# Optimization experiments

Measured on AMD Instinct MI355X. Metric: run time of the kernel, lower is better.

The kernel has to match this reference:

```python
import jax, jax.numpy as jnp
import numpy as np
import math

BS, S, D = 1, 2048, 1024
H = 16
DK = D // H  # 64


def _log_sparse_neighbor_mask(seq_len):
    """mask[i,j]=True iff j==i, or j in [i-k, i) with k=seq_len//2, or i-j is a power of 2.
    Matches generate_log_sparse_plus_neighbors_mask(seq_len, seq_len//2)."""
    k = seq_len // 2
    i = jnp.arange(seq_len, dtype=jnp.int32)[:, None]
    j = jnp.arange(seq_len, dtype=jnp.int32)[None, :]
    diff = i - j
    neighbor = (diff >= 0) & (diff <= k)  # includes diagonal (diff==0)
    pow2 = (diff > 0) & ((diff & (diff - 1)) == 0)
    return neighbor | pow2  # [seq_len, seq_len] bool


def setup_inputs() -> dict:
    key = jax.random.key(0)
    ks = jax.random.split(key, 9)
    std = 0.02
    return {
        "Q": jax.random.normal(ks[0], (BS, S, D), dtype=jnp.float32),
        "Wq": jax.random.normal(ks[1], (D, H * DK), dtype=jnp.float32) * std,
        "bq": jnp.zeros((H * DK,), dtype=jnp.float32),
        "Wk": jax.random.normal(ks[2], (D, H * DK), dtype=jnp.float32) * std,
        "bk": jnp.zeros((H * DK,), dtype=jnp.float32),
        "Wv": jax.random.normal(ks[3], (D, H * DK), dtype=jnp.float32) * std,
        "bv": jnp.zeros((H * DK,), dtype=jnp.float32),
        "Wo": jax.random.normal(ks[4], (H * DK, D), dtype=jnp.float32) * std,
        "bo": jnp.zeros((D,), dtype=jnp.float32),
    }


def reference(Q, Wq, bq, Wk, bk, Wv, bv, Wo, bo):
    bs, s, d = Q.shape
    # QKV projections -> [bs, h, s, dk]
    q = (Q @ Wq + bq).reshape(bs, s, H, DK).transpose(0, 2, 1, 3)
    k = (Q @ Wk + bk).reshape(bs, s, H, DK).transpose(0, 2, 1, 3)
    v = (Q @ Wv + bv).reshape(bs, s, H, DK).transpose(0, 2, 1, 3)

    # log_sparse_attention: scale is 1/sqrt(d_k); mask regenerated internally
    mask = _log_sparse_neighbor_mask(s)  # [s, s] bool
    scores = jnp.einsum("bhqd,bhkd->bhqk", q, k) / math.sqrt(DK)
    scores = jnp.where(mask[None, None, :, :], scores, -jnp.inf)
    attn = jax.nn.softmax(scores, axis=-1)  # [bs, h, s, s]
    out = jnp.einsum("bhqk,bhkd->bhqd", attn, v)

    # merge heads + output projection
    out = out.transpose(0, 2, 1, 3).reshape(bs, s, H * DK)
    out = out @ Wo + bo
    return (out, attn)
```

## Files before the change

### kernel.cpp

```cpp
#include <hip/hip_runtime.h>

#define SEQ 2048
#define DM 1024
#define NH 16
#define DKH 64
#define BAND 1024
#define QKV 3072
#define PBW 1064

typedef __attribute__((ext_vector_type(8))) __bf16 bf16x8;
typedef __attribute__((ext_vector_type(4))) __bf16 bf16x4;
typedef __attribute__((ext_vector_type(4))) float f32x4;

static __device__ __forceinline__ f32x4 mfma16(bf16x8 a, bf16x8 b, f32x4 c) {
  return __builtin_amdgcn_mfma_f32_16x16x32_bf16(a, b, c, 0, 0, 0);
}

#define GLOAD16(gp, lp)                                                        \
  __builtin_amdgcn_global_load_lds(                                            \
      (const __attribute__((address_space(1))) void*)(gp),                     \
      (__attribute__((address_space(3))) void*)(lp), 16, 0, 0)

struct PrepArgs {
  const float* win[4];
  __bf16* wout[4];
  const float* Q;
  __bf16* Qb;
};
__global__ void prep(PrepArgs P) {
  int z = blockIdx.z;
  if (z < 4) {
    __shared__ float t[32][33];
    const float* in = P.win[z];
    __bf16* out = P.wout[z];
    int c0 = blockIdx.x * 32, r0 = blockIdx.y * 32;
    int tx = threadIdx.x, ty = threadIdx.y;
    for (int r = ty; r < 32; r += 8)
      t[r][tx] = in[(size_t)(r0 + r) * DM + c0 + tx];
    __syncthreads();
    for (int r = ty; r < 32; r += 8)
      out[(size_t)(c0 + r) * DM + r0 + tx] = (__bf16)t[tx][r];
  } else {
    int t = threadIdx.y * 32 + threadIdx.x;
    int base = (blockIdx.y * 32 + blockIdx.x) * 512 + t;
#pragma unroll
    for (int u = 0; u < 2; u++) {
      int i = base + u * 256;
      float4 v = reinterpret_cast<const float4*>(P.Q)[i];
      bf16x4 o = {(__bf16)v.x, (__bf16)v.y, (__bf16)v.z, (__bf16)v.w};
      reinterpret_cast<bf16x4*>(P.Qb)[i] = o;
    }
  }
}

template <int BM, int BN, bool BF16OUT, bool VOUT>
__global__ __launch_bounds__(256) void gemm_lds(
    const __bf16* __restrict__ A, const __bf16* __restrict__ BT,
    const float* __restrict__ b0, const float* __restrict__ b1,
    const float* __restrict__ b2, float* __restrict__ Cf,
    __bf16* __restrict__ Cb, __bf16* __restrict__ VT, int M, int N, int K) {
  constexpr int BK = 64;
  constexpr int FM = BM / 32;
  constexpr int FN = BN / 32;
  constexpr int LA = BM * BK * 2 / (256 * 16);
  constexpr int LB = BN * BK * 2 / (256 * 16);
  __shared__ __bf16 lA[2][BM * BK];
  __shared__ __bf16 lB[2][BN * BK];
  int tid = threadIdx.x;
  int lane = tid & 63;
  int l15 = lane & 15, lg = lane >> 4;
  int w = tid >> 6;
  int nwg = gridDim.x * gridDim.y;
  int bid = blockIdx.y * gridDim.x + blockIdx.x;
  int swz = (bid & 7) * (nwg >> 3) + (bid >> 3);
  int bx = swz % gridDim.x;
  int by = swz / gridDim.x;
  int row0 = by * BM;
  int col0 = bx * BN;
  int sec = col0 >> 10;
  const float* bias = sec == 0 ? b0 : (sec == 1 ? b1 : b2);
  int cbase = col0 & (DM - 1);
  int wr = (w >> 1) * (BM / 2);
  int wc = (w & 1) * (BN / 2);
  f32x4 acc[FM][FN] = {};

  auto stage = [&](int b, int kt) {
#pragma unroll
    for (int s = 0; s < LA; s++) {
      int u = tid + s * 256;
      int r = u >> 3;
      int cc = (u & 7) ^ (r & 7);
      GLOAD16(A + (size_t)(row0 + r) * K + kt * BK + cc * 8,
              (char*)lA[b] + u * 16);
    }
#pragma unroll
    for (int s = 0; s < LB; s++) {
      int u = tid + s * 256;
      int r = u >> 3;
      int cc = (u & 7) ^ (r & 7);
      GLOAD16(BT + (size_t)(col0 + r) * K + kt * BK + cc * 8,
              (char*)lB[b] + u * 16);
    }
  };

  const int T = K / BK;
  stage(0, 0);
  stage(1, 1);
  for (int t = 0; t < T; t++) {
    if (t + 1 < T)
      asm volatile("s_waitcnt vmcnt(%0)" ::"i"(LA + LB) : "memory");
    else
      asm volatile("s_waitcnt vmcnt(0)" ::: "memory");
    __builtin_amdgcn_s_barrier();
    int cur = t & 1;
    bf16x8 af[2][FM], bfr[2][FN];
#pragma unroll
    for (int kh = 0; kh < 2; kh++) {
#pragma unroll
      for (int mi = 0; mi < FM; mi++) {
        int r = wr + mi * 16 + l15;
        af[kh][mi] = *(const bf16x8*)((const char*)lA[cur] + r * 128 +
                                      ((((kh << 2) | lg) ^ (r & 7)) << 4));
      }
#pragma unroll
      for (int ni = 0; ni < FN; ni++) {
        int r = wc + ni * 16 + l15;
        bfr[kh][ni] = *(const bf16x8*)((const char*)lB[cur] + r * 128 +
                                       ((((kh << 2) | lg) ^ (r & 7)) << 4));
      }
    }
    __builtin_amdgcn_s_setprio(1);
#pragma unroll
    for (int kh = 0; kh < 2; kh++)
#pragma unroll
      for (int mi = 0; mi < FM; mi++)
#pragma unroll
        for (int ni = 0; ni < FN; ni++)
          acc[mi][ni] = mfma16(af[kh][mi], bfr[kh][ni], acc[mi][ni]);
    __builtin_amdgcn_s_setprio(0);
    __builtin_amdgcn_s_barrier();
    if (t + 2 < T) stage(cur, t + 2);
  }

  if (VOUT && sec == 2) {
#pragma unroll
    for (int mi = 0; mi < FM; mi++) {
      int row = row0 + wr + mi * 16 + lg * 4;
#pragma unroll
      for (int ni = 0; ni < FN; ni++) {
        int hd = cbase + wc + ni * 16 + l15;
        float b = bias[hd];
        bf16x4 pk;
#pragma unroll
        for (int r = 0; r < 4; r++) pk[r] = (__bf16)(acc[mi][ni][r] + b);
        *(bf16x4*)&VT[(size_t)hd * SEQ + row] = pk;
      }
    }
    return;
  }
#pragma unroll
  for (int mi = 0; mi < FM; mi++) {
    int row = row0 + wr + mi * 16 + lg * 4;
#pragma unroll
    for (int ni = 0; ni < FN; ni++) {
      int col = col0 + wc + ni * 16 + l15;
      float b = bias[(cbase + wc + ni * 16 + l15) & (DM - 1)];
#pragma unroll
      for (int r = 0; r < 4; r++) {
        float v = acc[mi][ni][r] + b;
        if constexpr (BF16OUT)
          Cb[(size_t)(row + r) * N + col] = (__bf16)v;
        else
          Cf[(size_t)(row + r) * N + col] = v;
      }
    }
  }
}

__global__ __launch_bounds__(256, 4) void attn_fused(
    const __bf16* __restrict__ qkvb, const __bf16* __restrict__ VT,
    float* __restrict__ attn_out, __bf16* __restrict__ pvb) {
  __shared__ __bf16 pbuf[16][PBW];
  __shared__ float wsum[4][16];
  __shared__ float sinv[16];

  int nwg = gridDim.x * gridDim.y;
  int bid = blockIdx.y * gridDim.x + blockIdx.x;
  int swz = (bid & 7) * (nwg >> 3) + (bid >> 3);
  int h = swz / (SEQ / 16);
  int i0 = (swz % (SEQ / 16)) * 16;

  int tid = threadIdx.x, lane = tid & 63, w = tid >> 6;
  int l15 = lane & 15, lg = lane >> 4;

  int jlo = i0 - BAND;
  if (jlo < 0) jlo = 0;
  int ntiles = (i0 + 16 - jlo) >> 4;
  int ktiles = (ntiles + 1) & ~1;
  int n = ntiles * 16;

  const __bf16* qptr = qkvb + (size_t)(i0 + l15) * QKV + h * DKH + lg * 8;
  bf16x8 aq0 = *(const bf16x8*)qptr;
  bf16x8 aq1 = *(const bf16x8*)(qptr + 32);
  const __bf16* kbase = qkvb + DM + h * DKH + lg * 8;

  float sm[4] = {0.f, 0.f, 0.f, 0.f};
  for (int t = w; t < ntiles; t += 4) {
    int jb = jlo + t * 16;
    const __bf16* kptr = kbase + (size_t)(jb + l15) * QKV;
    f32x4 acc = {0.f, 0.f, 0.f, 0.f};
    __builtin_amdgcn_s_setprio(1);
    acc = mfma16(aq0, *(const bf16x8*)kptr, acc);
    acc = mfma16(aq1, *(const bf16x8*)(kptr + 32), acc);
    __builtin_amdgcn_s_setprio(0);
    int col = jb + l15;
    int x = jb - jlo + l15;
#pragma unroll
    for (int r = 0; r < 4; r++) {
      int i = i0 + lg * 4 + r;
      float e = 0.f;
      if (col <= i && i - col <= BAND) {
        e = __expf(acc[r] * 0.125f);
        sm[r] += e;
      }
      pbuf[lg * 4 + r][x] = (__bf16)e;
    }
  }
  if (ktiles != ntiles) pbuf[tid >> 4][n + (tid & 15)] = (__bf16)0.f;
#pragma unroll
  for (int o = 1; o < 16; o <<= 1)
#pragma unroll
    for (int r = 0; r < 4; r++) sm[r] += __shfl_xor(sm[r], o);
  if (l15 == 0)
#pragma unroll
    for (int r = 0; r < 4; r++) wsum[w][lg * 4 + r] = sm[r];
  __syncthreads();
  if (tid < 16)
    sinv[tid] = 1.f / (wsum[0][tid] + wsum[1][tid] + wsum[2][tid] + wsum[3][tid]);
  __syncthreads();

  f32x4* abase = (f32x4*)(attn_out + ((size_t)h * SEQ + i0) * SEQ);
  for (int idx = tid; idx < 16 * (SEQ / 4); idx += 256) {
    int row = idx >> 9;
    int j4 = idx & 511;
    int x = j4 * 4 - jlo;
    bool valid = (unsigned)x < (unsigned)n;
    int xc = valid ? x : 0;
    bf16x4 v4 = *(const bf16x4*)&pbuf[row][xc];
    float inv = valid ? sinv[row] : 0.f;
    f32x4 o = {(float)v4[0] * inv, (float)v4[1] * inv, (float)v4[2] * inv,
               (float)v4[3] * inv};
    __builtin_nontemporal_store(o, abase + idx);
  }

  f32x4 acc = {0.f, 0.f, 0.f, 0.f};
  int d0 = w * 16;
  const __bf16* vtp = VT + ((size_t)h * DKH + d0 + l15) * SEQ;
  for (int kt = 0; kt < ktiles; kt += 2) {
    int kk = kt * 16;
    bf16x8 pa = *(const bf16x8*)&pbuf[l15][kk + lg * 8];
    int jj = jlo + kk + lg * 8;
    bf16x8 vf = {};
    if (jj < SEQ) vf = *(const bf16x8*)(vtp + jj);
    __builtin_amdgcn_s_setprio(1);
    acc = mfma16(pa, vf, acc);
    __builtin_amdgcn_s_setprio(0);
  }
#pragma unroll
  for (int r = 0; r < 4; r++) {
    int row = lg * 4 + r;
    float inv = sinv[row];
    pvb[(size_t)(i0 + row) * DM + h * DKH + d0 + l15] = (__bf16)(acc[r] * inv);
  }
}

extern "C" void kernel_launch(void* const* d_in, const int* in_sizes, int n_in,
                              void* d_out, int out_size, void* d_ws,
                              size_t ws_size, hipStream_t stream) {
  const float* Q = (const float*)d_in[0];
  const float* Wq = (const float*)d_in[1];
  const float* bq = (const float*)d_in[2];
  const float* Wk = (const float*)d_in[3];
  const float* bk = (const float*)d_in[4];
  const float* Wv = (const float*)d_in[5];
  const float* bv = (const float*)d_in[6];
  const float* Wo = (const float*)d_in[7];
  const float* bo = (const float*)d_in[8];
  float* out_proj = (float*)d_out;
  float* attn_out = out_proj + (size_t)SEQ * DM;

  char* ws = (char*)d_ws;
  size_t off = 0;
  auto alloc = [&](size_t bytes) {
    void* p = ws + off;
    off = (off + bytes + 255) & ~(size_t)255;
    return p;
  };
  __bf16* Qb    = (__bf16*)alloc((size_t)SEQ * DM * 2);
  __bf16* WqkvT = (__bf16*)alloc((size_t)QKV * DM * 2);
  __bf16* WoT   = (__bf16*)alloc((size_t)DM * DM * 2);
  __bf16* qkvb  = (__bf16*)alloc((size_t)SEQ * QKV * 2);
  __bf16* VT    = (__bf16*)alloc((size_t)NH * DKH * SEQ * 2);
  __bf16* pvb   = (__bf16*)alloc((size_t)SEQ * DM * 2);

  PrepArgs P;
  P.win[0] = Wq; P.win[1] = Wk; P.win[2] = Wv; P.win[3] = Wo;
  P.wout[0] = WqkvT;
  P.wout[1] = WqkvT + (size_t)DM * DM;
  P.wout[2] = WqkvT + (size_t)2 * DM * DM;
  P.wout[3] = WoT;
  P.Q = Q;
  P.Qb = Qb;
  prep<<<dim3(32, 32, 5), dim3(32, 8), 0, stream>>>(P);

  gemm_lds<64, 128, true, true><<<dim3(QKV / 128, SEQ / 64), 256, 0, stream>>>(
      Qb, WqkvT, bq, bk, bv, nullptr, qkvb, VT, SEQ, QKV, DM);

  attn_fused<<<dim3(SEQ / 16, NH), 256, 0, stream>>>(qkvb, VT, attn_out, pvb);

  gemm_lds<64, 64, false, false><<<dim3(DM / 64, SEQ / 64), 256, 0, stream>>>(
      pvb, WoT, bo, bo, bo, out_proj, nullptr, nullptr, SEQ, DM, DM);
}
```

Measured before the change: 119.7 us.

## Transpose QK MFMA for vector P stores and interleave attn write with PV

```diff
diff --git a/kernel.cpp b/kernel.cpp
--- a/kernel.cpp
+++ b/kernel.cpp
@@ -204,67 +204,64 @@
   bf16x8 aq1 = *(const bf16x8*)(qptr + 32);
   const __bf16* kbase = qkvb + DM + h * DKH + lg * 8;
 
-  float sm[4] = {0.f, 0.f, 0.f, 0.f};
+  int i = i0 + l15;
+  float sm = 0.f;
   for (int t = w; t < ntiles; t += 4) {
     int jb = jlo + t * 16;
     const __bf16* kptr = kbase + (size_t)(jb + l15) * QKV;
     f32x4 acc = {0.f, 0.f, 0.f, 0.f};
     __builtin_amdgcn_s_setprio(1);
-    acc = mfma16(aq0, *(const bf16x8*)kptr, acc);
-    acc = mfma16(aq1, *(const bf16x8*)(kptr + 32), acc);
+    acc = mfma16(*(const bf16x8*)kptr, aq0, acc);
+    acc = mfma16(*(const bf16x8*)(kptr + 32), aq1, acc);
     __builtin_amdgcn_s_setprio(0);
-    int col = jb + l15;
-    int x = jb - jlo + l15;
+    int kcol = jb + lg * 4;
+    bf16x4 pk;
 #pragma unroll
     for (int r = 0; r < 4; r++) {
-      int i = i0 + lg * 4 + r;
+      int j = kcol + r;
       float e = 0.f;
-      if (col <= i && i - col <= BAND) {
-        e = __expf(acc[r] * 0.125f);
-        sm[r] += e;
-      }
-      pbuf[lg * 4 + r][x] = (__bf16)e;
-    }
+      if (j <= i && i - j <= BAND) {
+        e = exp2f(acc[r] * 0.18033688f);
+        sm += e;
+      }
+      pk[r] = (__bf16)e;
+    }
+    *(bf16x4*)&pbuf[l15][jb - jlo + lg * 4] = pk;
   }
   if (ktiles != ntiles) pbuf[tid >> 4][n + (tid & 15)] = (__bf16)0.f;
-#pragma unroll
-  for (int o = 1; o < 16; o <<= 1)
-#pragma unroll
-    for (int r = 0; r < 4; r++) sm[r] += __shfl_xor(sm[r], o);
-  if (l15 == 0)
-#pragma unroll
-    for (int r = 0; r < 4; r++) wsum[w][lg * 4 + r] = sm[r];
+  sm += __shfl_xor(sm, 16);
+  sm += __shfl_xor(sm, 32);
+  if (lane < 16) wsum[w][lane] = sm;
   __syncthreads();
   if (tid < 16)
     sinv[tid] = 1.f / (wsum[0][tid] + wsum[1][tid] + wsum[2][tid] + wsum[3][tid]);
   __syncthreads();
 
   f32x4* abase = (f32x4*)(attn_out + ((size_t)h * SEQ + i0) * SEQ);
-  for (int idx = tid; idx < 16 * (SEQ / 4); idx += 256) {
-    int row = idx >> 9;
-    int j4 = idx & 511;
-    int x = j4 * 4 - jlo;
-    bool valid = (unsigned)x < (unsigned)n;
-    int xc = valid ? x : 0;
-    bf16x4 v4 = *(const bf16x4*)&pbuf[row][xc];
-    float inv = valid ? sinv[row] : 0.f;
-    f32x4 o = {(float)v4[0] * inv, (float)v4[1] * inv, (float)v4[2] * inv,
-               (float)v4[3] * inv};
-    __builtin_nontemporal_store(o, abase + idx);
-  }
-
   f32x4 acc = {0.f, 0.f, 0.f, 0.f};
   int d0 = w * 16;
   const __bf16* vtp = VT + ((size_t)h * DKH + d0 + l15) * SEQ;
-  for (int kt = 0; kt < ktiles; kt += 2) {
-    int kk = kt * 16;
-    bf16x8 pa = *(const bf16x8*)&pbuf[l15][kk + lg * 8];
-    int jj = jlo + kk + lg * 8;
-    bf16x8 vf = {};
-    if (jj < SEQ) vf = *(const bf16x8*)(vtp + jj);
-    __builtin_amdgcn_s_setprio(1);
-    acc = mfma16(pa, vf, acc);
-    __builtin_amdgcn_s_setprio(0);
+  for (int s = 0; s < 33; s++) {
+    if (s < 32) {
+      int idx = tid + s * 256;
+      int row = idx >> 9;
+      int j4 = idx & 511;
+      int x = j4 * 4 - jlo;
+      bool valid = (unsigned)x < (unsigned)n;
+      bf16x4 v4 = *(const bf16x4*)&pbuf[row][valid ? x : 0];
+      float inv = valid ? sinv[row] : 0.f;
+      f32x4 o = {(float)v4[0] * inv, (float)v4[1] * inv, (float)v4[2] * inv,
+                 (float)v4[3] * inv};
+      __builtin_nontemporal_store(o, abase + idx);
+    }
+    if (2 * s < ktiles) {
+      int kk = s * 32;
+      bf16x8 pa = *(const bf16x8*)&pbuf[l15][kk + lg * 8];
+      int jj = jlo + kk + lg * 8;
+      bf16x8 vf = {};
+      if (jj < SEQ) vf = *(const bf16x8*)(vtp + jj);
+      acc = mfma16(pa, vf, acc);
+    }
   }
 #pragma unroll
   for (int r = 0; r < 4; r++) {
```

After: 120.9 us. No clear change (+1.0%).

## Process 32 query rows per attention block to reuse K and V tiles

Applied to the files above, without the earlier changes.

```diff
diff --git a/kernel.cpp b/kernel.cpp
--- a/kernel.cpp
+++ b/kernel.cpp
@@ -6,6 +6,7 @@
 #define DKH 64
 #define BAND 1024
 #define QKV 3072
+#define QBLK 32
 #define PBW 1064
 
 typedef __attribute__((ext_vector_type(8))) __bf16 bf16x8;
@@ -177,70 +178,90 @@
   }
 }
 
-__global__ __launch_bounds__(256, 4) void attn_fused(
+__global__ __launch_bounds__(256, 2) void attn_fused(
     const __bf16* __restrict__ qkvb, const __bf16* __restrict__ VT,
     float* __restrict__ attn_out, __bf16* __restrict__ pvb) {
-  __shared__ __bf16 pbuf[16][PBW];
-  __shared__ float wsum[4][16];
-  __shared__ float sinv[16];
+  __shared__ __bf16 pbuf[QBLK][PBW];
+  __shared__ float wsum[4][QBLK];
+  __shared__ float sinv[QBLK];
 
   int nwg = gridDim.x * gridDim.y;
   int bid = blockIdx.y * gridDim.x + blockIdx.x;
   int swz = (bid & 7) * (nwg >> 3) + (bid >> 3);
-  int h = swz / (SEQ / 16);
-  int i0 = (swz % (SEQ / 16)) * 16;
+  int h = swz / (SEQ / QBLK);
+  int i0 = (swz % (SEQ / QBLK)) * QBLK;
 
   int tid = threadIdx.x, lane = tid & 63, w = tid >> 6;
   int l15 = lane & 15, lg = lane >> 4;
 
   int jlo = i0 - BAND;
   if (jlo < 0) jlo = 0;
-  int ntiles = (i0 + 16 - jlo) >> 4;
-  int ktiles = (ntiles + 1) & ~1;
+  int ntiles = (i0 + QBLK - jlo) >> 4;
   int n = ntiles * 16;
 
-  const __bf16* qptr = qkvb + (size_t)(i0 + l15) * QKV + h * DKH + lg * 8;
-  bf16x8 aq0 = *(const bf16x8*)qptr;
-  bf16x8 aq1 = *(const bf16x8*)(qptr + 32);
+  const __bf16* qptr0 = qkvb + (size_t)(i0 + l15) * QKV + h * DKH + lg * 8;
+  const __bf16* qptr1 = qptr0 + (size_t)16 * QKV;
+  bf16x8 aq0 = *(const bf16x8*)qptr0;
+  bf16x8 aq1 = *(const bf16x8*)(qptr0 + 32);
+  bf16x8 aq2 = *(const bf16x8*)qptr1;
+  bf16x8 aq3 = *(const bf16x8*)(qptr1 + 32);
   const __bf16* kbase = qkvb + DM + h * DKH + lg * 8;
 
-  float sm[4] = {0.f, 0.f, 0.f, 0.f};
+  float sm0[4] = {0.f, 0.f, 0.f, 0.f};
+  float sm1[4] = {0.f, 0.f, 0.f, 0.f};
   for (int t = w; t < ntiles; t += 4) {
     int jb = jlo + t * 16;
     const __bf16* kptr = kbase + (size_t)(jb + l15) * QKV;
-    f32x4 acc = {0.f, 0.f, 0.f, 0.f};
+    bf16x8 k0 = *(const bf16x8*)kptr;
+    bf16x8 k1 = *(const bf16x8*)(kptr + 32);
+    f32x4 acc0 = {0.f, 0.f, 0.f, 0.f};
+    f32x4 acc1 = {0.f, 0.f, 0.f, 0.f};
     __builtin_amdgcn_s_setprio(1);
-    acc = mfma16(aq0, *(const bf16x8*)kptr, acc);
-    acc = mfma16(aq1, *(const bf16x8*)(kptr + 32), acc);
+    acc0 = mfma16(aq0, k0, acc0);
+    acc0 = mfma16(aq1, k1, acc0);
+    acc1 = mfma16(aq2, k0, acc1);
+    acc1 = mfma16(aq3, k1, acc1);
     __builtin_amdgcn_s_setprio(0);
     int col = jb + l15;
     int x = jb - jlo + l15;
 #pragma unroll
     for (int r = 0; r < 4; r++) {
       int i = i0 + lg * 4 + r;
-      float e = 0.f;
+      float e0 = 0.f;
       if (col <= i && i - col <= BAND) {
-        e = __expf(acc[r] * 0.125f);
-        sm[r] += e;
-      }
-      pbuf[lg * 4 + r][x] = (__bf16)e;
-    }
-  }
-  if (ktiles != ntiles) pbuf[tid >> 4][n + (tid & 15)] = (__bf16)0.f;
+        e0 = __expf(acc0[r] * 0.125f);
+        sm0[r] += e0;
+      }
+      pbuf[lg * 4 + r][x] = (__bf16)e0;
+      int i2 = i + 16;
+      float e1 = 0.f;
+      if (col <= i2 && i2 - col <= BAND) {
+        e1 = __expf(acc1[r] * 0.125f);
+        sm1[r] += e1;
+      }
+      pbuf[16 + lg * 4 + r][x] = (__bf16)e1;
+    }
+  }
 #pragma unroll
   for (int o = 1; o < 16; o <<= 1)
 #pragma unroll
-    for (int r = 0; r < 4; r++) sm[r] += __shfl_xor(sm[r], o);
+    for (int r = 0; r < 4; r++) {
+      sm0[r] += __shfl_xor(sm0[r], o);
+      sm1[r] += __shfl_xor(sm1[r], o);
+    }
   if (l15 == 0)
 #pragma unroll
-    for (int r = 0; r < 4; r++) wsum[w][lg * 4 + r] = sm[r];
+    for (int r = 0; r < 4; r++) {
+      wsum[w][lg * 4 + r] = sm0[r];
+      wsum[w][16 + lg * 4 + r] = sm1[r];
+    }
   __syncthreads();
-  if (tid < 16)
+  if (tid < QBLK)
     sinv[tid] = 1.f / (wsum[0][tid] + wsum[1][tid] + wsum[2][tid] + wsum[3][tid]);
   __syncthreads();
 
   f32x4* abase = (f32x4*)(attn_out + ((size_t)h * SEQ + i0) * SEQ);
-  for (int idx = tid; idx < 16 * (SEQ / 4); idx += 256) {
+  for (int idx = tid; idx < QBLK * (SEQ / 4); idx += 256) {
     int row = idx >> 9;
     int j4 = idx & 511;
     int x = j4 * 4 - jlo;
@@ -253,24 +274,27 @@
     __builtin_nontemporal_store(o, abase + idx);
   }
 
-  f32x4 acc = {0.f, 0.f, 0.f, 0.f};
+  f32x4 acc0 = {0.f, 0.f, 0.f, 0.f};
+  f32x4 acc1 = {0.f, 0.f, 0.f, 0.f};
   int d0 = w * 16;
   const __bf16* vtp = VT + ((size_t)h * DKH + d0 + l15) * SEQ;
-  for (int kt = 0; kt < ktiles; kt += 2) {
+  for (int kt = 0; kt < ntiles; kt += 2) {
     int kk = kt * 16;
-    bf16x8 pa = *(const bf16x8*)&pbuf[l15][kk + lg * 8];
-    int jj = jlo + kk + lg * 8;
-    bf16x8 vf = {};
-    if (jj < SEQ) vf = *(const bf16x8*)(vtp + jj);
+    bf16x8 pa0 = *(const bf16x8*)&pbuf[l15][kk + lg * 8];
+    bf16x8 pa1 = *(const bf16x8*)&pbuf[16 + l15][kk + lg * 8];
+    bf16x8 vf = *(const bf16x8*)(vtp + jlo + kk + lg * 8);
     __builtin_amdgcn_s_setprio(1);
-    acc = mfma16(pa, vf, acc);
+    acc0 = mfma16(pa0, vf, acc0);
+    acc1 = mfma16(pa1, vf, acc1);
     __builtin_amdgcn_s_setprio(0);
   }
 #pragma unroll
   for (int r = 0; r < 4; r++) {
     int row = lg * 4 + r;
-    float inv = sinv[row];
-    pvb[(size_t)(i0 + row) * DM + h * DKH + d0 + l15] = (__bf16)(acc[r] * inv);
+    pvb[(size_t)(i0 + row) * DM + h * DKH + d0 + l15] =
+        (__bf16)(acc0[r] * sinv[row]);
+    pvb[(size_t)(i0 + 16 + row) * DM + h * DKH + d0 + l15] =
+        (__bf16)(acc1[r] * sinv[16 + row]);
   }
 }
 
@@ -316,7 +340,7 @@
   gemm_lds<64, 128, true, true><<<dim3(QKV / 128, SEQ / 64), 256, 0, stream>>>(
       Qb, WqkvT, bq, bk, bv, nullptr, qkvb, VT, SEQ, QKV, DM);
 
-  attn_fused<<<dim3(SEQ / 16, NH), 256, 0, stream>>>(qkvb, VT, attn_out, pvb);
+  attn_fused<<<dim3(SEQ / QBLK, NH), 256, 0, stream>>>(qkvb, VT, attn_out, pvb);
 
   gemm_lds<64, 64, false, false><<<dim3(DM / 64, SEQ / 64), 256, 0, stream>>>(
       pvb, WoT, bo, bo, bo, out_proj, nullptr, nullptr, SEQ, DM, DM);
```

Result: faster. 116.1 us (median of 2 runs) (-3.0%).
